# Optimization experiments

Measured on AMD Instinct MI355X. Metric: run time of the kernel, lower is better.

The kernel has to match this reference:

```python
import jax, jax.numpy as jnp
import numpy as np

D = 256
H = 4
HD = D // H


def setup_inputs() -> dict:
    key = jax.random.key(0)
    ks = jax.random.split(key, 12)
    A, T = 64, 512
    s = 1.0 / np.sqrt(D)
    return {
        "features": jax.random.normal(ks[0], (A, T, D), jnp.float32),
        "positions": jax.random.normal(ks[1], (A, T, 2), jnp.float32),
        "Wq": jax.random.normal(ks[2], (D, D), jnp.float32) * s,
        "bq": jnp.zeros((D,), jnp.float32),
        "Wk": jax.random.normal(ks[3], (D, D), jnp.float32) * s,
        "bk": jnp.zeros((D,), jnp.float32),
        "Wv": jax.random.normal(ks[4], (D, D), jnp.float32) * s,
        "bv": jnp.zeros((D,), jnp.float32),
        "Wo": jax.random.normal(ks[5], (D, D), jnp.float32) * s,
        "bo": jnp.zeros((D,), jnp.float32),
        "max_distance": 2,
        "time_window": 64,
    }


def _sparse_mask(positions, max_distance, time_window):
    # positions: [A, T, 2] -> allowed [A, T, T]
    A, T, _ = positions.shape
    diff = positions[:, :, None, :] - positions[:, None, :, :]  # [A,T,T,2]
    dist2 = jnp.sum(diff * diff, axis=-1)                       # [A,T,T]
    t = jnp.arange(T)
    tmask = jnp.abs(t[:, None] - t[None, :]) <= time_window      # [T,T]
    return (dist2 <= float(max_distance) ** 2) & tmask[None]     # [A,T,T]


def reference(features, positions, Wq, bq, Wk, bk, Wv, bv, Wo, bo,
              max_distance, time_window):
    A, T, Dm = features.shape
    allowed = _sparse_mask(positions, max_distance, time_window)  # [A,T,T]
    q = features @ Wq.T + bq
    k = features @ Wk.T + bk
    v = features @ Wv.T + bv
    # split heads: [A, T, H, HD]
    q = q.reshape(A, T, H, HD)
    k = k.reshape(A, T, H, HD)
    v = v.reshape(A, T, H, HD)
    scale = 1.0 / np.sqrt(HD)
    scores = jnp.einsum("athd,ashd->ahts", q, k) * scale          # [A,H,T,T]
    scores = jnp.where(allowed[:, None], scores, -jnp.inf)
    attn = jax.nn.softmax(scores, axis=-1)
    out = jnp.einsum("ahts,ashd->athd", attn, v).reshape(A, T, Dm)
    return out @ Wo.T + bo
```

## Files before the change

### kernel.cpp

```cpp
#include <hip/hip_runtime.h>
#include <hip/hip_bf16.h>
#include <cstdint>
#include <cstddef>

typedef __attribute__((ext_vector_type(8))) _Float16 half8;
typedef __attribute__((ext_vector_type(4))) _Float16 half4v;
typedef __attribute__((ext_vector_type(4))) float floatx4;

#define MFMA16(a, b, c) __builtin_amdgcn_mfma_f32_16x16x32_f16((a), (b), (c), 0, 0, 0)

#define GLOAD_LDS16(g, l)                                                     \
    __builtin_amdgcn_global_load_lds(                                         \
        (const __attribute__((address_space(1))) void*)(g),                   \
        (__attribute__((address_space(3))) void*)(l), 16, 0, 0)

#define NFEAT 8388608
#define NW    65536

__global__ __launch_bounds__(256) void convert_kernel(
    const float* __restrict__ feat, const float* __restrict__ wq,
    const float* __restrict__ wk, const float* __restrict__ wv,
    const float* __restrict__ wo, _Float16* __restrict__ out)
{
    long tid  = (long)blockIdx.x * blockDim.x + threadIdx.x;
    long base = tid * 4;
    if (base >= (long)NFEAT + 4L * NW) return;
    const float* src;
    long off;
    if (base < NFEAT) { src = feat; off = base; }
    else {
        long r = base - NFEAT;
        int  w = (int)(r >> 16);
        off = r & (NW - 1);
        src = (w == 0) ? wq : (w == 1) ? wk : (w == 2) ? wv : wo;
    }
    float4 v = *(const float4*)(src + off);
    half4v h = { (_Float16)v.x, (_Float16)v.y, (_Float16)v.z, (_Float16)v.w };
    *(half4v*)(out + base) = h;
}


__device__ __forceinline__ void stage128x64(
    const _Float16* __restrict__ src, _Float16* __restrict__ lds,
    int wid, int lane)
{
#pragma unroll
    for (int i = 0; i < 4; ++i) {
        int grp = wid * 4 + i;
        int row = grp * 8 + (lane >> 3);
        int sc  = (lane & 7) ^ (row & 7);
        GLOAD_LDS16(src + (size_t)row * 256 + sc * 8, lds + grp * 512);
    }
}

template <bool OUT_HALF>
__device__ __forceinline__ void gemm128x128(
    const _Float16* __restrict__ X, const _Float16* __restrict__ W,
    const float* __restrict__ bias, void* __restrict__ Cptr, int bm, int bn)
{
    __shared__ _Float16 As[128 * 64];
    __shared__ _Float16 Bs[128 * 64];

    const int tid  = threadIdx.x;
    const int lane = tid & 63, wid = tid >> 6;
    const int quad = lane >> 4, l16 = lane & 15;
    const int wm = wid & 1, wn = wid >> 1;

    floatx4 acc[4][4] = {};
    const _Float16* Xg = X + (size_t)bm * 128 * 256;
    const _Float16* Wg = W + (size_t)bn * 128 * 256;

    for (int k0 = 0; k0 < 256; k0 += 64) {
        stage128x64(Xg + k0, As, wid, lane);
        stage128x64(Wg + k0, Bs, wid, lane);
        __syncthreads();
#pragma unroll
        for (int kh = 0; kh < 2; ++kh) {
            half8 af[4], bf[4];
#pragma unroll
            for (int mi = 0; mi < 4; ++mi) {
                int row = wm * 64 + mi * 16 + l16;
                int ch  = (kh * 4 + quad) ^ (l16 & 7);
                af[mi] = *(const half8*)(&As[row * 64 + ch * 8]);
            }
#pragma unroll
            for (int ni = 0; ni < 4; ++ni) {
                int row = wn * 64 + ni * 16 + l16;
                int ch  = (kh * 4 + quad) ^ (l16 & 7);
                bf[ni] = *(const half8*)(&Bs[row * 64 + ch * 8]);
            }
#pragma unroll
            for (int mi = 0; mi < 4; ++mi)
#pragma unroll
                for (int ni = 0; ni < 4; ++ni)
                    acc[mi][ni] = MFMA16(af[mi], bf[ni], acc[mi][ni]);
        }
        __syncthreads();
    }

#pragma unroll
    for (int ni = 0; ni < 4; ++ni) {
        int col = bn * 128 + wn * 64 + ni * 16 + l16;
        float bv = bias[col];
#pragma unroll
        for (int mi = 0; mi < 4; ++mi) {
#pragma unroll
            for (int r = 0; r < 4; ++r) {
                int row = bm * 128 + wm * 64 + mi * 16 + quad * 4 + r;
                float v = acc[mi][ni][r] + bv;
                if (OUT_HALF)
                    ((_Float16*)Cptr)[(size_t)row * 256 + col] = (_Float16)v;
                else
                    ((float*)Cptr)[(size_t)row * 256 + col] = v;
            }
        }
    }
}

__global__ __launch_bounds__(256) void qkv_gemm(
    const _Float16* __restrict__ featH, const _Float16* __restrict__ WH,
    const float* __restrict__ bq, const float* __restrict__ bk,
    const float* __restrict__ bv,
    _Float16* __restrict__ Qb, _Float16* __restrict__ Kb, _Float16* __restrict__ Vb)
{
    int z = blockIdx.x >> 1, bn = blockIdx.x & 1;
    const _Float16* W = WH + (size_t)z * NW;
    const float* bias = (z == 0) ? bq : (z == 1) ? bk : bv;
    _Float16* out    = (z == 0) ? Qb : (z == 1) ? Kb : Vb;
    gemm128x128<true>(featH, W, bias, out, blockIdx.y, bn);
}

__global__ __launch_bounds__(256) void out_gemm(
    const _Float16* __restrict__ attnH, const _Float16* __restrict__ WoH,
    const float* __restrict__ bo, float* __restrict__ out)
{
    gemm128x128<false>(attnH, WoH, bo, out, blockIdx.y, blockIdx.x);
}

__global__ __launch_bounds__(256) void attn_kernel(
    const _Float16* __restrict__ Qb, const _Float16* __restrict__ Kb,
    const _Float16* __restrict__ Vb, const float* __restrict__ positions,
    const int* __restrict__ mdp, const int* __restrict__ twp,
    _Float16* __restrict__ attnb)
{
    const int qt = blockIdx.x, h = blockIdx.y, a = blockIdx.z;
    const int q0 = qt * 64;
    const int s_base = q0 - 64;
    const int tid = threadIdx.x, lane = tid & 63, wid = tid >> 6;
    const int quad = lane >> 4, l16 = lane & 15;

    __shared__ _Float16 KPs[192 * 72];
    __shared__ _Float16 Vt[64 * 200];

    const size_t abase = (size_t)a * 512;

    const size_t qrow = abase + q0 + wid * 16 + l16;
    half8 aq0 = *(const half8*)(Qb + qrow * 256 + h * 64 + quad * 8);
    half8 aq1 = *(const half8*)(Qb + qrow * 256 + h * 64 + 32 + quad * 8);
    float qpx[4], qpy[4];
    int trow[4];
#pragma unroll
    for (int r = 0; r < 4; ++r) {
        int m = wid * 16 + quad * 4 + r;
        trow[r] = q0 + m;
        float2 qp = *(const float2*)(positions + (abase + q0 + m) * 2);
        qpx[r] = qp.x;
        qpy[r] = qp.y;
    }

#pragma unroll
    for (int i = 0; i < 6; ++i) {
        int c  = tid + 256 * i;
        int si = c >> 3, col = (c & 7) * 8;
        int sc = min(max(s_base + si, 0), 511);
        *(half8*)(&KPs[si * 72 + col]) =
            *(const half8*)(Kb + (abase + sc) * 256 + h * 64 + col);
    }
#pragma unroll
    for (int i = 0; i < 6; ++i) {
        int c  = tid + 256 * i;
        int si = c % 192;
        int d0 = (c / 192) * 8;
        int sc = min(max(s_base + si, 0), 511);
        half8 v = *(const half8*)(Vb + (abase + sc) * 256 + h * 64 + d0);
#pragma unroll
        for (int j = 0; j < 8; ++j) Vt[(d0 + j) * 200 + si] = v[j];
    }
    __syncthreads();

    const int md = *mdp, tw = *twp;
    const float md2 = (float)(md * md);

    floatx4 S[12];
#pragma unroll
    for (int j = 0; j < 12; ++j) {
        half8 bk0 = *(const half8*)(&KPs[(j * 16 + l16) * 72 + quad * 8]);
        half8 bk1 = *(const half8*)(&KPs[(j * 16 + l16) * 72 + 32 + quad * 8]);
        floatx4 acc = {};
        acc = MFMA16(aq0, bk0, acc);
        acc = MFMA16(aq1, bk1, acc);
        int si = j * 16 + l16;
        int sr = s_base + si;
        int sc = min(max(sr, 0), 511);
        float2 kp = *(const float2*)(positions + (abase + sc) * 2);
        bool svalid = (sr >= 0) && (sr < 512);
#pragma unroll
        for (int r = 0; r < 4; ++r) {
            float dx = qpx[r] - kp.x, dy = qpy[r] - kp.y;
            float d2 = dx * dx + dy * dy;
            int dt = trow[r] - sr; dt = dt < 0 ? -dt : dt;
            bool ok = svalid && (d2 <= md2) && (dt <= tw);
            S[j][r] = ok ? acc[r] * 0.125f : -1e30f;
        }
    }

    float minv[4];
#pragma unroll
    for (int r = 0; r < 4; ++r) {
        float m = -1e30f;
#pragma unroll
        for (int j = 0; j < 12; ++j) m = fmaxf(m, S[j][r]);
        m = fmaxf(m, __shfl_xor(m, 1));
        m = fmaxf(m, __shfl_xor(m, 2));
        m = fmaxf(m, __shfl_xor(m, 4));
        m = fmaxf(m, __shfl_xor(m, 8));
        float l = 0.f;
#pragma unroll
        for (int j = 0; j < 12; ++j) {
            float p = __expf(S[j][r] - m);
            S[j][r] = p;
            l += p;
        }
        l += __shfl_xor(l, 1);
        l += __shfl_xor(l, 2);
        l += __shfl_xor(l, 4);
        l += __shfl_xor(l, 8);
        minv[r] = 1.0f / l;
    }

    __syncthreads();

    _Float16* Ps = KPs + wid * 16 * 200;
#pragma unroll
    for (int j = 0; j < 12; ++j)
#pragma unroll
        for (int r = 0; r < 4; ++r)
            Ps[(quad * 4 + r) * 200 + j * 16 + l16] = (_Float16)(S[j][r] * minv[r]);

    half8 af[6];
#pragma unroll
    for (int k = 0; k < 6; ++k)
        af[k] = *(const half8*)(&Ps[l16 * 200 + k * 32 + quad * 8]);
#pragma unroll
    for (int n = 0; n < 4; ++n) {
        floatx4 accO = {};
#pragma unroll
        for (int k = 0; k < 6; ++k) {
            half8 bv = *(const half8*)(&Vt[(n * 16 + l16) * 200 + k * 32 + quad * 8]);
            accO = MFMA16(af[k], bv, accO);
        }
#pragma unroll
        for (int r = 0; r < 4; ++r) {
            int row = q0 + wid * 16 + quad * 4 + r;
            attnb[(abase + row) * 256 + h * 64 + n * 16 + l16] = (_Float16)accO[r];
        }
    }
}

extern "C" void kernel_launch(void* const* d_in, const int* in_sizes, int n_in,
                              void* d_out, int out_size, void* d_ws, size_t ws_size,
                              hipStream_t stream)
{
    const float* feat = (const float*)d_in[0];
    const float* pos  = (const float*)d_in[1];
    const float* Wq   = (const float*)d_in[2];
    const float* bq   = (const float*)d_in[3];
    const float* Wk   = (const float*)d_in[4];
    const float* bk   = (const float*)d_in[5];
    const float* Wv   = (const float*)d_in[6];
    const float* bv   = (const float*)d_in[7];
    const float* Wo   = (const float*)d_in[8];
    const float* bo   = (const float*)d_in[9];
    const int*   md   = (const int*)d_in[10];
    const int*   tw   = (const int*)d_in[11];
    float*       out  = (float*)d_out;

    _Float16* ws    = (_Float16*)d_ws;
    _Float16* featH = ws;
    _Float16* WH    = featH + NFEAT;
    _Float16* Qb    = WH + 4 * NW;
    _Float16* Kb    = Qb + NFEAT;
    _Float16* Vb    = Kb + NFEAT;
    _Float16* attnH = featH;

    convert_kernel<<<8448, 256, 0, stream>>>(feat, Wq, Wk, Wv, Wo, ws);

    dim3 gqkv(6, 256);
    qkv_gemm<<<gqkv, 256, 0, stream>>>(featH, WH, bq, bk, bv, Qb, Kb, Vb);

    dim3 gattn(8, 4, 64);
    attn_kernel<<<gattn, 256, 0, stream>>>(Qb, Kb, Vb, pos, md, tw, attnH);

    dim3 gout(2, 256);
    out_gemm<<<gout, 256, 0, stream>>>(attnH, WH + 3 * (size_t)NW, bo, out);
}
```

Before: 183.6 us.

## Fuse fp32-to-fp16 conversion into GEMM staging and swizzle attention LDS

```diff
diff --git a/kernel.cpp b/kernel.cpp
--- a/kernel.cpp
+++ b/kernel.cpp
@@ -4,7 +4,6 @@
 #include <cstddef>
 
 typedef __attribute__((ext_vector_type(8))) _Float16 half8;
-typedef __attribute__((ext_vector_type(4))) _Float16 half4v;
 typedef __attribute__((ext_vector_type(4))) float floatx4;
 
 #define MFMA16(a, b, c) __builtin_amdgcn_mfma_f32_16x16x32_f16((a), (b), (c), 0, 0, 0)
@@ -15,32 +14,9 @@
         (__attribute__((address_space(3))) void*)(l), 16, 0, 0)
 
 #define NFEAT 8388608
-#define NW    65536
-
-__global__ __launch_bounds__(256) void convert_kernel(
-    const float* __restrict__ feat, const float* __restrict__ wq,
-    const float* __restrict__ wk, const float* __restrict__ wv,
-    const float* __restrict__ wo, _Float16* __restrict__ out)
-{
-    long tid  = (long)blockIdx.x * blockDim.x + threadIdx.x;
-    long base = tid * 4;
-    if (base >= (long)NFEAT + 4L * NW) return;
-    const float* src;
-    long off;
-    if (base < NFEAT) { src = feat; off = base; }
-    else {
-        long r = base - NFEAT;
-        int  w = (int)(r >> 16);
-        off = r & (NW - 1);
-        src = (w == 0) ? wq : (w == 1) ? wk : (w == 2) ? wv : wo;
-    }
-    float4 v = *(const float4*)(src + off);
-    half4v h = { (_Float16)v.x, (_Float16)v.y, (_Float16)v.z, (_Float16)v.w };
-    *(half4v*)(out + base) = h;
-}
-
-
-__device__ __forceinline__ void stage128x64(
+
+
+__device__ __forceinline__ void stage_dma(
     const _Float16* __restrict__ src, _Float16* __restrict__ lds,
     int wid, int lane)
 {
@@ -53,9 +29,26 @@
     }
 }
 
-template <bool OUT_HALF>
+__device__ __forceinline__ void stage_f32(
+    const float* __restrict__ src, _Float16* __restrict__ lds, int tid)
+{
+#pragma unroll
+    for (int i = 0; i < 4; ++i) {
+        int g   = tid + 256 * i;
+        int row = g >> 3, chd = g & 7;
+        int chs = chd ^ (row & 7);
+        const float* s = src + (size_t)row * 256 + chs * 8;
+        float4 v0 = *(const float4*)s;
+        float4 v1 = *(const float4*)(s + 4);
+        half8 h = { (_Float16)v0.x, (_Float16)v0.y, (_Float16)v0.z, (_Float16)v0.w,
+                    (_Float16)v1.x, (_Float16)v1.y, (_Float16)v1.z, (_Float16)v1.w };
+        *(half8*)(&lds[row * 64 + chd * 8]) = h;
+    }
+}
+
+template <bool XF32, bool OUT_HALF>
 __device__ __forceinline__ void gemm128x128(
-    const _Float16* __restrict__ X, const _Float16* __restrict__ W,
+    const void* __restrict__ Xv, const float* __restrict__ Wf,
     const float* __restrict__ bias, void* __restrict__ Cptr, int bm, int bn)
 {
     __shared__ _Float16 As[128 * 64];
@@ -67,12 +60,14 @@
     const int wm = wid & 1, wn = wid >> 1;
 
     floatx4 acc[4][4] = {};
-    const _Float16* Xg = X + (size_t)bm * 128 * 256;
-    const _Float16* Wg = W + (size_t)bn * 128 * 256;
+    const float* Wg = Wf + (size_t)bn * 128 * 256;
 
     for (int k0 = 0; k0 < 256; k0 += 64) {
-        stage128x64(Xg + k0, As, wid, lane);
-        stage128x64(Wg + k0, Bs, wid, lane);
+        if (XF32)
+            stage_f32(((const float*)Xv) + (size_t)bm * 128 * 256 + k0, As, tid);
+        else
+            stage_dma(((const _Float16*)Xv) + (size_t)bm * 128 * 256 + k0, As, wid, lane);
+        stage_f32(Wg + k0, Bs, tid);
         __syncthreads();
 #pragma unroll
         for (int kh = 0; kh < 2; ++kh) {
@@ -118,23 +113,25 @@
 }
 
 __global__ __launch_bounds__(256) void qkv_gemm(
-    const _Float16* __restrict__ featH, const _Float16* __restrict__ WH,
+    const float* __restrict__ feat,
+    const float* __restrict__ Wq, const float* __restrict__ Wk,
+    const float* __restrict__ Wv,
     const float* __restrict__ bq, const float* __restrict__ bk,
     const float* __restrict__ bv,
     _Float16* __restrict__ Qb, _Float16* __restrict__ Kb, _Float16* __restrict__ Vb)
 {
     int z = blockIdx.x >> 1, bn = blockIdx.x & 1;
-    const _Float16* W = WH + (size_t)z * NW;
+    const float* W    = (z == 0) ? Wq : (z == 1) ? Wk : Wv;
     const float* bias = (z == 0) ? bq : (z == 1) ? bk : bv;
-    _Float16* out    = (z == 0) ? Qb : (z == 1) ? Kb : Vb;
-    gemm128x128<true>(featH, W, bias, out, blockIdx.y, bn);
+    _Float16* out     = (z == 0) ? Qb : (z == 1) ? Kb : Vb;
+    gemm128x128<true, true>(feat, W, bias, out, blockIdx.y, bn);
 }
 
 __global__ __launch_bounds__(256) void out_gemm(
-    const _Float16* __restrict__ attnH, const _Float16* __restrict__ WoH,
+    const _Float16* __restrict__ attnH, const float* __restrict__ Wo,
     const float* __restrict__ bo, float* __restrict__ out)
 {
-    gemm128x128<false>(attnH, WoH, bo, out, blockIdx.y, blockIdx.x);
+    gemm128x128<false, false>(attnH, Wo, bo, out, blockIdx.y, blockIdx.x);
 }
 
 __global__ __launch_bounds__(256) void attn_kernel(
@@ -149,10 +146,12 @@
     const int tid = threadIdx.x, lane = tid & 63, wid = tid >> 6;
     const int quad = lane >> 4, l16 = lane & 15;
 
-    __shared__ _Float16 KPs[192 * 72];
-    __shared__ _Float16 Vt[64 * 200];
+    __shared__ _Float16 KPs[192 * 64];
+    __shared__ _Float16 Vt[64 * 196];
 
     const size_t abase = (size_t)a * 512;
+    const int md = *mdp, tw = *twp;
+    const float md2 = (float)(md * md);
 
     const size_t qrow = abase + q0 + wid * 16 + l16;
     half8 aq0 = *(const half8*)(Qb + qrow * 256 + h * 64 + quad * 8);
@@ -170,36 +169,39 @@
 
 #pragma unroll
     for (int i = 0; i < 6; ++i) {
-        int c  = tid + 256 * i;
-        int si = c >> 3, col = (c & 7) * 8;
-        int sc = min(max(s_base + si, 0), 511);
-        *(half8*)(&KPs[si * 72 + col]) =
-            *(const half8*)(Kb + (abase + sc) * 256 + h * 64 + col);
-    }
-#pragma unroll
-    for (int i = 0; i < 6; ++i) {
-        int c  = tid + 256 * i;
-        int si = c % 192;
-        int d0 = (c / 192) * 8;
-        int sc = min(max(s_base + si, 0), 511);
-        half8 v = *(const half8*)(Vb + (abase + sc) * 256 + h * 64 + d0);
-#pragma unroll
-        for (int j = 0; j < 8; ++j) Vt[(d0 + j) * 200 + si] = v[j];
+        int grp = wid * 6 + i;
+        int si  = grp * 8 + (lane >> 3);
+        int sc  = min(max(s_base + si, 0), 511);
+        int ch  = (lane & 7) ^ (si & 7);
+        GLOAD_LDS16(Kb + (abase + sc) * 256 + h * 64 + ch * 8, KPs + grp * 512);
+    }
+#pragma unroll
+    for (int i = 0; i < 3; ++i) {
+        int idx = tid + 256 * i;
+        int si2 = (idx % 96) * 2;
+        int d0  = (idx / 96) * 8;
+        int sa  = min(max(s_base + si2, 0), 511);
+        int sb  = min(max(s_base + si2 + 1, 0), 511);
+        half8 v0 = *(const half8*)(Vb + (abase + sa) * 256 + h * 64 + d0);
+        half8 v1 = *(const half8*)(Vb + (abase + sb) * 256 + h * 64 + d0);
+#pragma unroll
+        for (int j = 0; j < 8; ++j) {
+            union { _Float16 hh[2]; uint32_t u; } p;
+            p.hh[0] = v0[j]; p.hh[1] = v1[j];
+            *(uint32_t*)(&Vt[(d0 + j) * 196 + si2]) = p.u;
+        }
     }
     __syncthreads();
 
-    const int md = *mdp, tw = *twp;
-    const float md2 = (float)(md * md);
-
     floatx4 S[12];
 #pragma unroll
     for (int j = 0; j < 12; ++j) {
-        half8 bk0 = *(const half8*)(&KPs[(j * 16 + l16) * 72 + quad * 8]);
-        half8 bk1 = *(const half8*)(&KPs[(j * 16 + l16) * 72 + 32 + quad * 8]);
+        int si = j * 16 + l16;
+        half8 bk0 = *(const half8*)(&KPs[si * 64 + ((quad) ^ (si & 7)) * 8]);
+        half8 bk1 = *(const half8*)(&KPs[si * 64 + ((4 + quad) ^ (si & 7)) * 8]);
         floatx4 acc = {};
         acc = MFMA16(aq0, bk0, acc);
         acc = MFMA16(aq1, bk1, acc);
-        int si = j * 16 + l16;
         int sr = s_base + si;
         int sc = min(max(sr, 0), 511);
         float2 kp = *(const float2*)(positions + (abase + sc) * 2);
@@ -240,23 +242,29 @@
 
     __syncthreads();
 
-    _Float16* Ps = KPs + wid * 16 * 200;
+    _Float16* Ps = KPs + wid * (16 * 192);
 #pragma unroll
     for (int j = 0; j < 12; ++j)
 #pragma unroll
-        for (int r = 0; r < 4; ++r)
-            Ps[(quad * 4 + r) * 200 + j * 16 + l16] = (_Float16)(S[j][r] * minv[r]);
+        for (int r = 0; r < 4; ++r) {
+            int row = quad * 4 + r;
+            int col = j * 16 + l16;
+            int ch  = (col >> 3) ^ (row & 7);
+            Ps[row * 192 + ch * 8 + (col & 7)] = (_Float16)(S[j][r] * minv[r]);
+        }
 
     half8 af[6];
 #pragma unroll
-    for (int k = 0; k < 6; ++k)
-        af[k] = *(const half8*)(&Ps[l16 * 200 + k * 32 + quad * 8]);
+    for (int k = 0; k < 6; ++k) {
+        int ch = (k * 4 + quad) ^ (l16 & 7);
+        af[k] = *(const half8*)(&Ps[l16 * 192 + ch * 8]);
+    }
 #pragma unroll
     for (int n = 0; n < 4; ++n) {
         floatx4 accO = {};
 #pragma unroll
         for (int k = 0; k < 6; ++k) {
-            half8 bv = *(const half8*)(&Vt[(n * 16 + l16) * 200 + k * 32 + quad * 8]);
+            half8 bv = *(const half8*)(&Vt[(n * 16 + l16) * 196 + k * 32 + quad * 8]);
             accO = MFMA16(af[k], bv, accO);
         }
 #pragma unroll
@@ -286,21 +294,17 @@
     float*       out  = (float*)d_out;
 
     _Float16* ws    = (_Float16*)d_ws;
-    _Float16* featH = ws;
-    _Float16* WH    = featH + NFEAT;
-    _Float16* Qb    = WH + 4 * NW;
+    _Float16* Qb    = ws;
     _Float16* Kb    = Qb + NFEAT;
     _Float16* Vb    = Kb + NFEAT;
-    _Float16* attnH = featH;
-
-    convert_kernel<<<8448, 256, 0, stream>>>(feat, Wq, Wk, Wv, Wo, ws);
+    _Float16* attnH = Vb + NFEAT;
 
     dim3 gqkv(6, 256);
-    qkv_gemm<<<gqkv, 256, 0, stream>>>(featH, WH, bq, bk, bv, Qb, Kb, Vb);
+    qkv_gemm<<<gqkv, 256, 0, stream>>>(feat, Wq, Wk, Wv, bq, bk, bv, Qb, Kb, Vb);
 
     dim3 gattn(8, 4, 64);
     attn_kernel<<<gattn, 256, 0, stream>>>(Qb, Kb, Vb, pos, md, tw, attnH);
 
     dim3 gout(2, 256);
-    out_gemm<<<gout, 256, 0, stream>>>(attnH, WH + 3 * (size_t)NW, bo, out);
-}
+    out_gemm<<<gout, 256, 0, stream>>>(attnH, Wo, bo, out);
+}
```

Result: slower. 193.5 us (+5.4%).
